# Performance work log

Measured on AMD Instinct MI355X. Metric: run time of the kernel, lower is better.

The kernel has to match this reference:

```python
import jax, jax.numpy as jnp
import numpy as np
from jax import lax

NUM_EXPERTS = 5
K = 3


def setup_inputs() -> dict:
    key = jax.random.key(0)
    ks = jax.random.split(key, 16)
    B = 8192
    d_in, d_h = 32 * 10 * 10, 128

    def w(k, shape, fan_in):
        return jax.random.normal(k, shape, jnp.float32) / np.sqrt(fan_in)

    return {
        "x": jax.random.normal(ks[0], (B, 1, 28, 28), jnp.float32),
        # conv feature extractor: 28 -> conv5 -> 24 -> pool2 -> 12 -> conv3 -> 10
        "conv1_w": w(ks[1], (16, 1, 5, 5), 25),
        "conv1_b": jnp.zeros((16,), jnp.float32),
        "conv2_w": w(ks[2], (32, 16, 3, 3), 16 * 9),
        "conv2_b": jnp.zeros((32,), jnp.float32),
        # top-k gate
        "gate_w": w(ks[3], (d_in, NUM_EXPERTS), d_in),
        "gate_b": jnp.zeros((NUM_EXPERTS,), jnp.float32),
        # 5 experts: Linear(3200,128)-Tanh-Linear(128,128)-Tanh, stacked on axis 0
        "e1_w": w(ks[4], (NUM_EXPERTS, d_in, d_h), d_in),
        "e1_b": jnp.zeros((NUM_EXPERTS, d_h), jnp.float32),
        "e2_w": w(ks[5], (NUM_EXPERTS, d_h, d_h), d_h),
        "e2_b": jnp.zeros((NUM_EXPERTS, d_h), jnp.float32),
        # softmax head
        "sm_w": w(ks[6], (d_h, 10), d_h),
        "sm_b": jnp.zeros((10,), jnp.float32),
    }


def _conv_features(x, c1w, c1b, c2w, c2b):
    dn = ("NCHW", "OIHW", "NCHW")
    h = lax.conv_general_dilated(x, c1w, (1, 1), "VALID", dimension_numbers=dn)
    h = jax.nn.relu(h + c1b[None, :, None, None])          # [B,16,24,24]
    h = lax.reduce_window(h, -jnp.inf, lax.max, (1, 1, 2, 2), (1, 1, 2, 2), "VALID")  # [B,16,12,12]
    h = lax.conv_general_dilated(h, c2w, (1, 1), "VALID", dimension_numbers=dn)
    h = jax.nn.relu(h + c2b[None, :, None, None])          # [B,32,10,10]
    return h.reshape(h.shape[0], -1)                       # [B,3200]


def reference(x, conv1_w, conv1_b, conv2_w, conv2_b, gate_w, gate_b,
              e1_w, e1_b, e2_w, e2_b, sm_w, sm_b):
    h = _conv_features(x, conv1_w, conv1_b, conv2_w, conv2_b)  # [B, 3200]
    B = h.shape[0]

    # token-choice top-K gating over NUM_EXPERTS experts
    probs = jax.nn.softmax(h @ gate_w + gate_b, axis=-1)       # [B, E]
    topv, topi = lax.top_k(probs, K)                           # [B, K]
    topv = topv / jnp.sum(topv, axis=-1, keepdims=True)        # renormalize
    w_full = jnp.zeros((B, NUM_EXPERTS), h.dtype).at[
        jnp.arange(B)[:, None], topi].set(topv)                # [B, E] sparse combine weights

    # expert MLPs (small, computed densely and masked by gate weights)
    h1 = jnp.tanh(jnp.einsum("bd,edh->ebh", h, e1_w) + e1_b[:, None, :])   # [E,B,128]
    h2 = jnp.tanh(jnp.einsum("ebh,ehk->ebk", h1, e2_w) + e2_b[:, None, :])  # [E,B,128]
    moe_out = jnp.einsum("be,ebk->bk", w_full, h2)             # weighted sum combine, [B,128]

    logits = moe_out @ sm_w + sm_b                             # [B,10]
    return jax.nn.softmax(logits, axis=1)
```

## Files before the change

### kernel.cpp

```cpp
#include <hip/hip_runtime.h>
#include <hip/hip_bf16.h>
#include <hip/hip_fp16.h>

#define NB 8192
#define D_IN 3200
#define D_H 128
#define NE 5

typedef _Float16 f16x8 __attribute__((ext_vector_type(8)));
typedef _Float16 f16x4 __attribute__((ext_vector_type(4)));
typedef float f32x4 __attribute__((ext_vector_type(4)));

__device__ __forceinline__ void gload16(const _Float16* g, _Float16* l) {
    __builtin_amdgcn_global_load_lds(
        (const __attribute__((address_space(1))) void*)g,
        (__attribute__((address_space(3))) void*)l, 16, 0, 0);
}

__global__ __launch_bounds__(256) void k_gwprep(const float* __restrict__ gw,
                                                float* __restrict__ gwC,
                                                int* __restrict__ cnt) {
    int i = blockIdx.x * 256 + threadIdx.x;
    if (i < 16000) {
        int e = i / 3200, rem = i - e * 3200;
        int o = rem >> 5, co = rem & 31;
        gwC[i] = gw[(co * 100 + o) * 5 + e];
    }
    if (blockIdx.x == 0 && threadIdx.x < NE) cnt[threadIdx.x] = 0;
}

#define PCL_S 24
__global__ __launch_bounds__(256, 3) void k_feat(
    const float* __restrict__ x, const float* __restrict__ c1w, const float* __restrict__ c1b,
    const float* __restrict__ c2w, const float* __restrict__ c2b,
    const float* __restrict__ gwC, const float* __restrict__ gb,
    const float* __restrict__ e1w, _Float16* __restrict__ wT,
    const float* __restrict__ e2w, _Float16* __restrict__ e2T,
    _Float16* __restrict__ h16, float* __restrict__ wfull)
{
    __shared__ union {
        struct {
            __align__(16) float xs[784];
            __align__(16) float c1wsP[448];
            __align__(16) _Float16 b2h[5120];
            __align__(16) _Float16 b2l[5120];
            __align__(16) _Float16 pclh[144 * PCL_S];
            __align__(16) _Float16 pcll[144 * PCL_S];
            float red[32];
        } f;
        float tile[64 * 65];
    } S;
    int bid = blockIdx.x;
    int t = threadIdx.x;

    if (bid < 520) {
        if (bid < 500) {
            int e = bid / 100, rem = bid - e * 100;
            int k0 = (rem >> 1) * 64, n0 = (rem & 1) * 64;
            const float* src = e1w + (size_t)e * D_IN * D_H;
            _Float16* dst = wT + (size_t)e * D_H * D_IN;
            for (int i = 0; i < 16; ++i) {
                int idx = t + i * 256;
                int kr = idx >> 6, nc = idx & 63;
                S.tile[kr * 65 + nc] = src[(size_t)(k0 + kr) * D_H + n0 + nc];
            }
            __syncthreads();
            for (int i = 0; i < 16; ++i) {
                int idx = t + i * 256;
                int nr = idx >> 6, kc = idx & 63;
                dst[(size_t)(n0 + nr) * D_IN + k0 + kc] = (_Float16)S.tile[kc * 65 + nr];
            }
        } else {
            int idx2 = bid - 500;
            int e = idx2 >> 2, rem = idx2 & 3;
            int k0 = (rem >> 1) * 64, n0 = (rem & 1) * 64;
            const float* src = e2w + (size_t)e * D_H * D_H;
            _Float16* dst = e2T + (size_t)e * D_H * D_H;
            for (int i = 0; i < 16; ++i) {
                int idx = t + i * 256;
                int kr = idx >> 6, nc = idx & 63;
                S.tile[kr * 65 + nc] = src[(size_t)(k0 + kr) * D_H + n0 + nc];
            }
            __syncthreads();
            for (int i = 0; i < 16; ++i) {
                int idx = t + i * 256;
                int nr = idx >> 6, kc = idx & 63;
                dst[(size_t)(n0 + nr) * D_H + k0 + kc] = (_Float16)S.tile[kc * 65 + nr];
            }
        }
        return;
    }

    int b = bid - 520;
    for (int i = t; i < 784; i += 256) S.f.xs[i] = x[(size_t)b * 784 + i];
    for (int i = t; i < 400; i += 256) {
        int c = i / 25, q = i - c * 25;
        S.f.c1wsP[c * 28 + q] = c1w[i];
    }
    for (int i = t; i < 5120; i += 256) {
        int co = i / 160, k = i - co * 160;
        int s = k >> 4, ci = k & 15;
        float v = (s == 9) ? 0.f : c2w[(co * 16 + ci) * 9 + s];
        _Float16 vh = (_Float16)v;
        S.f.b2h[i] = vh;
        S.f.b2l[i] = (_Float16)(v - (float)vh);
    }
    __syncthreads();

    {
        int c = t >> 4;
        int tile = t & 15;
        int tr = tile >> 2, tc = tile & 3;
        float w1r[25];
        #pragma unroll
        for (int q = 0; q < 6; ++q) {
            float4 v4 = *(const float4*)&S.f.c1wsP[c * 28 + q * 4];
            w1r[q * 4 + 0] = v4.x; w1r[q * 4 + 1] = v4.y;
            w1r[q * 4 + 2] = v4.z; w1r[q * 4 + 3] = v4.w;
        }
        w1r[24] = S.f.c1wsP[c * 28 + 24];
        float bias1 = c1b[c];
        float win[5][10];
        float pacc[3][3];
        #pragma unroll
        for (int i = 0; i < 3; ++i)
            #pragma unroll
            for (int j = 0; j < 3; ++j) pacc[i][j] = 0.f;
        int r0 = 6 * tr, col0 = 6 * tc;
        #pragma unroll
        for (int cr = 0; cr < 6; ++cr) {
            if (cr == 0) {
                #pragma unroll
                for (int rr = 0; rr < 5; ++rr)
                    #pragma unroll
                    for (int m = 0; m < 5; ++m) {
                        float2 v = *(const float2*)&S.f.xs[(r0 + rr) * 28 + col0 + 2 * m];
                        win[rr][2 * m] = v.x; win[rr][2 * m + 1] = v.y;
                    }
            } else {
                int dstr = (cr + 4) % 5;
                #pragma unroll
                for (int m = 0; m < 5; ++m) {
                    float2 v = *(const float2*)&S.f.xs[(r0 + cr + 4) * 28 + col0 + 2 * m];
                    win[dstr][2 * m] = v.x; win[dstr][2 * m + 1] = v.y;
                }
            }
            #pragma unroll
            for (int oc = 0; oc < 6; ++oc) {
                float s = bias1;
                #pragma unroll
                for (int u = 0; u < 5; ++u)
                    #pragma unroll
                    for (int v = 0; v < 5; ++v)
                        s += win[(cr + u) % 5][oc + v] * w1r[u * 5 + v];
                s = fmaxf(s, 0.f);
                pacc[cr >> 1][oc >> 1] = fmaxf(pacc[cr >> 1][oc >> 1], s);
            }
        }
        #pragma unroll
        for (int i = 0; i < 3; ++i)
            #pragma unroll
            for (int j = 0; j < 3; ++j) {
                int pos = (3 * tr + i) * 12 + (3 * tc + j);
                float v = pacc[i][j];
                _Float16 vh = (_Float16)v;
                S.f.pclh[pos * PCL_S + c] = vh;
                S.f.pcll[pos * PCL_S + c] = (_Float16)(v - (float)vh);
            }
    }
    __syncthreads();

    float part[5] = {0, 0, 0, 0, 0};
    int lane = t & 63, wv = t >> 6;
    int quad = lane >> 4, l16 = lane & 15;
    int quadh = quad >> 1, quadl = quad & 1;
    const int offA[5] = {0, 2, 13, 24, 26};
    const int offB[5] = {1, 12, 14, 25, 0};
    {
        int nt = wv & 1;
        int co = nt * 16 + l16;
        f16x8 bh[5], bl[5];
        #pragma unroll
        for (int kc = 0; kc < 5; ++kc) {
            bh[kc] = *(const f16x8*)&S.f.b2h[co * 160 + kc * 32 + quad * 8];
            bl[kc] = *(const f16x8*)&S.f.b2l[co * 160 + kc * 32 + quad * 8];
        }
        float bco = c2b[co];
        for (int mt = wv >> 1; mt < 7; mt += 2) {
            int o_a = mt * 16 + l16;
            int o_cl = o_a < 100 ? o_a : 99;
            int pb = (o_cl / 10) * 12 + (o_cl % 10);
            f32x4 acc = (f32x4){0.f, 0.f, 0.f, 0.f};
            #pragma unroll
            for (int kc = 0; kc < 5; ++kc) {
                int off = quadh ? offB[kc] : offA[kc];
                f16x8 ah = *(const f16x8*)&S.f.pclh[(pb + off) * PCL_S + quadl * 8];
                f16x8 al = *(const f16x8*)&S.f.pcll[(pb + off) * PCL_S + quadl * 8];
                acc = __builtin_amdgcn_mfma_f32_16x16x32_f16(ah, bh[kc], acc, 0, 0, 0);
                acc = __builtin_amdgcn_mfma_f32_16x16x32_f16(ah, bl[kc], acc, 0, 0, 0);
                acc = __builtin_amdgcn_mfma_f32_16x16x32_f16(al, bh[kc], acc, 0, 0, 0);
            }
            if (mt < 6 || quad == 0) {
                int o0 = mt * 16 + quad * 4;
                f16x4 st;
                #pragma unroll
                for (int r = 0; r < 4; ++r) {
                    float hv = fmaxf(acc[r] + bco, 0.f);
                    st[r] = (_Float16)hv;
                    #pragma unroll
                    for (int e = 0; e < 5; ++e)
                        part[e] += hv * gwC[e * 3200 + (o0 + r) * 32 + co];
                }
                *(f16x4*)&h16[(size_t)b * D_IN + co * 100 + o0] = st;
            }
        }
    }

    #pragma unroll
    for (int e = 0; e < 5; ++e) {
        float v = part[e];
        for (int off = 32; off > 0; off >>= 1) v += __shfl_down(v, off, 64);
        if (lane == 0) S.f.red[wv * 8 + e] = v;
    }
    __syncthreads();
    if (t == 0) {
        float lg[5], p[5];
        float mx = -1e30f;
        for (int e = 0; e < 5; ++e) {
            lg[e] = S.f.red[e] + S.f.red[8 + e] + S.f.red[16 + e] + S.f.red[24 + e] + gb[e];
            mx = fmaxf(mx, lg[e]);
        }
        float sum = 0.f;
        for (int e = 0; e < 5; ++e) { p[e] = expf(lg[e] - mx); sum += p[e]; }
        for (int e = 0; e < 5; ++e) p[e] /= sum;
        bool used[5] = {false, false, false, false, false};
        float out5[5] = {0, 0, 0, 0, 0};
        int ti[3]; float tv[3]; float tsum = 0.f;
        for (int jj = 0; jj < 3; ++jj) {
            int best = 0; float bv = -1.f;
            for (int e = 0; e < 5; ++e)
                if (!used[e] && p[e] > bv) { bv = p[e]; best = e; }
            used[best] = true; ti[jj] = best; tv[jj] = bv; tsum += bv;
        }
        for (int jj = 0; jj < 3; ++jj) out5[ti[jj]] = tv[jj] / tsum;
        for (int e = 0; e < 5; ++e) wfull[b * 5 + e] = out5[e];
    }
}

__global__ __launch_bounds__(256) void k_compact(
    const float* __restrict__ wfull, int* __restrict__ cnt, int* __restrict__ lists)
{
    int tok = blockIdx.x * 256 + threadIdx.x;
    int lane = threadIdx.x & 63;
    float w[5];
    #pragma unroll
    for (int e = 0; e < 5; ++e) w[e] = wfull[(size_t)tok * 5 + e];
    #pragma unroll
    for (int e = 0; e < 5; ++e) {
        bool sel = w[e] > 0.f;
        unsigned long long mask = __ballot(sel);
        int leader = __ffsll((long long)mask) - 1;
        int base = 0;
        if (lane == leader) base = atomicAdd(&cnt[e], __popcll(mask));
        base = __shfl(base, leader, 64);
        if (sel) {
            int pos = base + __popcll(mask & ((1ull << lane) - 1ull));
            lists[e * NB + pos] = tok;
        }
    }
}

#define H1S 136
union SLds {
    struct { _Float16 As0[2048]; _Float16 As1[2048];
             _Float16 Bs0[4096]; _Float16 Bs1[4096]; } p1;
    _Float16 e2ws[128 * H1S];
    _Float16 smwT[16 * 128];
};

__global__ __launch_bounds__(256, 3) void k_e1e2(
    const _Float16* __restrict__ h16, const _Float16* __restrict__ wT,
    const _Float16* __restrict__ e2T,
    const float* __restrict__ e1b, const float* __restrict__ e2b,
    const float* __restrict__ smw,
    const float* __restrict__ wfull, const int* __restrict__ cnt,
    const int* __restrict__ lists, float* __restrict__ logits)
{
    __shared__ SLds u;
    __shared__ __align__(16) _Float16 h1s[64 * H1S];
    __shared__ float wfl[64];
    __shared__ int rows[64];
    int bid = blockIdx.x;
    int e = bid >> 7;
    int mt = bid & 127;
    int cnt_e = cnt[e];
    int m0 = mt * 64;
    if (m0 >= cnt_e) return;
    int t = threadIdx.x;
    int lane = t & 63, wv = t >> 6;
    int waveM = wv >> 1, waveN = wv & 1;
    int quad = lane >> 4, l16 = lane & 15;
    if (t < 64) {
        int r = m0 + t;
        int row = (r < cnt_e) ? lists[e * NB + r] : lists[e * NB];
        rows[t] = row;
        wfl[t] = (r < cnt_e) ? wfull[(size_t)row * 5 + e] : 0.f;
    }
    __syncthreads();

    const _Float16* bbase = wT + (size_t)e * (D_H * D_IN);
    int srow = t >> 2;
    int scol = (t & 3) * 8;
    const _Float16* aptr = h16 + (size_t)rows[srow] * D_IN + scol;
    const _Float16* bptr0 = bbase + (size_t)srow * D_IN + scol;
    const _Float16* bptr1 = bbase + (size_t)(64 + srow) * D_IN + scol;
    f32x4 acc[2][4];
    #pragma unroll
    for (int i = 0; i < 2; ++i)
        #pragma unroll
        for (int j = 0; j < 4; ++j) acc[i][j] = (f32x4){0.f, 0.f, 0.f, 0.f};

    for (int k0 = 0; k0 < D_IN; k0 += 64) {
        gload16(aptr + k0,        u.p1.As0 + wv * 512);
        gload16(aptr + k0 + 32,   u.p1.As1 + wv * 512);
        gload16(bptr0 + k0,       u.p1.Bs0 + wv * 512);
        gload16(bptr0 + k0 + 32,  u.p1.Bs1 + wv * 512);
        gload16(bptr1 + k0,       u.p1.Bs0 + 2048 + wv * 512);
        gload16(bptr1 + k0 + 32,  u.p1.Bs1 + 2048 + wv * 512);
        __syncthreads();
        #pragma unroll
        for (int ch = 0; ch < 2; ++ch) {
            const _Float16* Ab = ch ? u.p1.As1 : u.p1.As0;
            const _Float16* Bb = ch ? u.p1.Bs1 : u.p1.Bs0;
            f16x8 af[2], bf[4];
            #pragma unroll
            for (int ms = 0; ms < 2; ++ms)
                af[ms] = *(const f16x8*)&Ab[(waveM * 32 + ms * 16 + l16) * 32 + quad * 8];
            #pragma unroll
            for (int ns = 0; ns < 4; ++ns)
                bf[ns] = *(const f16x8*)&Bb[(waveN * 64 + ns * 16 + l16) * 32 + quad * 8];
            #pragma unroll
            for (int ms = 0; ms < 2; ++ms)
                #pragma unroll
                for (int ns = 0; ns < 4; ++ns)
                    acc[ms][ns] = __builtin_amdgcn_mfma_f32_16x16x32_f16(af[ms], bf[ns], acc[ms][ns], 0, 0, 0);
        }
        __syncthreads();
    }

    #pragma unroll
    for (int ms = 0; ms < 2; ++ms) {
        int rbase = waveM * 32 + ms * 16 + quad * 4;
        #pragma unroll
        for (int ns = 0; ns < 4; ++ns) {
            int n = waveN * 64 + ns * 16 + l16;
            float bias = e1b[e * D_H + n];
            #pragma unroll
            for (int r = 0; r < 4; ++r)
                h1s[(rbase + r) * H1S + n] = (_Float16)tanhf(acc[ms][ns][r] + bias);
        }
    }
    __syncthreads();

    {
        int rr = t >> 1, cc = (t & 1) * 64;
        const _Float16* src = e2T + (size_t)e * (D_H * D_H) + (size_t)rr * D_H + cc;
        #pragma unroll
        for (int i = 0; i < 8; ++i)
            *(uint4*)&u.e2ws[rr * H1S + cc + i * 8] = *(const uint4*)(src + i * 8);
    }
    __syncthreads();

    f32x4 acc2[2][4];
    #pragma unroll
    for (int i = 0; i < 2; ++i)
        #pragma unroll
        for (int j = 0; j < 4; ++j) acc2[i][j] = (f32x4){0.f, 0.f, 0.f, 0.f};
    #pragma unroll
    for (int kc = 0; kc < 4; ++kc) {
        f16x8 a2[2], b2[4];
        #pragma unroll
        for (int ms = 0; ms < 2; ++ms)
            a2[ms] = *(const f16x8*)&h1s[(waveM * 32 + ms * 16 + l16) * H1S + kc * 32 + quad * 8];
        #pragma unroll
        for (int ns = 0; ns < 4; ++ns)
            b2[ns] = *(const f16x8*)&u.e2ws[(waveN * 64 + ns * 16 + l16) * H1S + kc * 32 + quad * 8];
        #pragma unroll
        for (int ms = 0; ms < 2; ++ms)
            #pragma unroll
            for (int ns = 0; ns < 4; ++ns)
                acc2[ms][ns] = __builtin_amdgcn_mfma_f32_16x16x32_f16(a2[ms], b2[ns], acc2[ms][ns], 0, 0, 0);
    }
    __syncthreads();

    for (int i = t; i < 2048; i += 256) {
        int n = i >> 7, k = i & 127;
        u.smwT[i] = (_Float16)(n < 10 ? smw[k * 10 + n] : 0.f);
    }
    #pragma unroll
    for (int ms = 0; ms < 2; ++ms) {
        int rbase = waveM * 32 + ms * 16 + quad * 4;
        #pragma unroll
        for (int ns = 0; ns < 4; ++ns) {
            int n = waveN * 64 + ns * 16 + l16;
            float bias = e2b[e * D_H + n];
            #pragma unroll
            for (int r = 0; r < 4; ++r) {
                int lrow = rbase + r;
                h1s[lrow * H1S + n] = (_Float16)(wfl[lrow] * tanhf(acc2[ms][ns][r] + bias));
            }
        }
    }
    __syncthreads();

    {
        f32x4 acc3 = (f32x4){0.f, 0.f, 0.f, 0.f};
        #pragma unroll
        for (int kc = 0; kc < 4; ++kc) {
            f16x8 a3 = *(const f16x8*)&h1s[(wv * 16 + l16) * H1S + kc * 32 + quad * 8];
            f16x8 b3 = *(const f16x8*)&u.smwT[l16 * 128 + kc * 32 + quad * 8];
            acc3 = __builtin_amdgcn_mfma_f32_16x16x32_f16(a3, b3, acc3, 0, 0, 0);
        }
        if (l16 < 10) {
            #pragma unroll
            for (int r = 0; r < 4; ++r) {
                int row = wv * 16 + quad * 4 + r;
                unsafeAtomicAdd(&logits[(size_t)rows[row] * 10 + l16], acc3[r]);
            }
        }
    }
}

__global__ __launch_bounds__(256) void k_smax(
    const float* __restrict__ logits, const float* __restrict__ smb,
    float* __restrict__ out)
{
    int r = blockIdx.x * 256 + threadIdx.x;
    float lg[10];
    float mx = -1e30f;
    #pragma unroll
    for (int c = 0; c < 10; ++c) {
        lg[c] = logits[(size_t)r * 10 + c] + smb[c];
        mx = fmaxf(mx, lg[c]);
    }
    float s = 0.f;
    #pragma unroll
    for (int c = 0; c < 10; ++c) { lg[c] = expf(lg[c] - mx); s += lg[c]; }
    float inv = 1.f / s;
    #pragma unroll
    for (int c = 0; c < 10; ++c) out[(size_t)r * 10 + c] = lg[c] * inv;
}

extern "C" void kernel_launch(void* const* d_in, const int* in_sizes, int n_in,
                              void* d_out, int out_size, void* d_ws, size_t ws_size,
                              hipStream_t stream)
{
    const float* x   = (const float*)d_in[0];
    const float* c1w = (const float*)d_in[1];
    const float* c1b = (const float*)d_in[2];
    const float* c2w = (const float*)d_in[3];
    const float* c2b = (const float*)d_in[4];
    const float* gw  = (const float*)d_in[5];
    const float* gb  = (const float*)d_in[6];
    const float* e1w = (const float*)d_in[7];
    const float* e1b = (const float*)d_in[8];
    const float* e2w = (const float*)d_in[9];
    const float* e2b = (const float*)d_in[10];
    const float* smw = (const float*)d_in[11];
    const float* smb = (const float*)d_in[12];
    float* out = (float*)d_out;

    char* ws = (char*)d_ws;
    size_t off = 0;
    auto alloc = [&](size_t bytes) {
        void* p = ws + off;
        off += (bytes + 255) & ~(size_t)255;
        return p;
    };
    _Float16* h16 = (_Float16*)alloc((size_t)NB * D_IN * 2);
    _Float16* wT  = (_Float16*)alloc((size_t)NE * D_H * D_IN * 2);
    _Float16* e2T = (_Float16*)alloc((size_t)NE * D_H * D_H * 2);
    float* wfull  = (float*)alloc((size_t)NB * NE * 4);
    float* logits = (float*)alloc((size_t)NB * 10 * 4);
    float* gwC    = (float*)alloc((size_t)NE * D_IN * 4);
    int* cnt      = (int*)alloc(NE * 4);
    int* lists    = (int*)alloc((size_t)NE * NB * 4);

    hipMemsetAsync(logits, 0, (size_t)NB * 10 * 4, stream);
    k_gwprep<<<dim3(63), 256, 0, stream>>>(gw, gwC, cnt);
    k_feat<<<dim3(520 + NB), 256, 0, stream>>>(x, c1w, c1b, c2w, c2b, gwC, gb,
                                               e1w, wT, e2w, e2T, h16, wfull);
    k_compact<<<dim3(NB / 256), 256, 0, stream>>>(wfull, cnt, lists);
    k_e1e2<<<dim3(128 * NE), 256, 0, stream>>>(h16, wT, e2T, e1b, e2b, smw,
                                               wfull, cnt, lists, logits);
    k_smax<<<dim3(NB / 256), 256, 0, stream>>>(logits, smb, out);
}
```

Baseline: 309.4 us.

## Precompute conv weight layouts once and shrink per-block LDS in feature kernel

New measurement: 346.1 us. 1.12x slower.

```diff
diff --git a/kernel.cpp b/kernel.cpp
--- a/kernel.cpp
+++ b/kernel.cpp
@@ -17,23 +17,42 @@
         (__attribute__((address_space(3))) void*)l, 16, 0, 0);
 }
 
-__global__ __launch_bounds__(256) void k_gwprep(const float* __restrict__ gw,
-                                                float* __restrict__ gwC,
-                                                int* __restrict__ cnt) {
+__global__ __launch_bounds__(256) void k_prep(const float* __restrict__ gw,
+                                              const float* __restrict__ c2w,
+                                              const float* __restrict__ c1w,
+                                              float* __restrict__ gwC8,
+                                              _Float16* __restrict__ b2g,
+                                              float* __restrict__ c1wP,
+                                              int* __restrict__ cnt) {
     int i = blockIdx.x * 256 + threadIdx.x;
-    if (i < 16000) {
-        int e = i / 3200, rem = i - e * 3200;
-        int o = rem >> 5, co = rem & 31;
-        gwC[i] = gw[(co * 100 + o) * 5 + e];
+    if (i < 25600) {
+        int idx = i >> 3, e = i & 7;
+        int o = idx >> 5, co = idx & 31;
+        gwC8[i] = (e < 5) ? gw[(co * 100 + o) * 5 + e] : 0.f;
+    } else if (i < 30720) {
+        int j = i - 25600;
+        int co = j / 160, k = j - co * 160;
+        int s = k >> 4, ci = k & 15;
+        float v = (s == 9) ? 0.f : c2w[(co * 16 + ci) * 9 + s];
+        _Float16 vh = (_Float16)v;
+        int kc = k >> 5, w = k & 31, quad = w >> 3, r = w & 7;
+        int base = ((co * 5 + kc) * 4 + quad) * 16 + r;
+        b2g[base] = vh;
+        b2g[base + 8] = (_Float16)(v - (float)vh);
+    } else if (i < 31120) {
+        int j = i - 30720;
+        int c = j / 25, q = j - c * 25;
+        c1wP[c * 28 + q] = c1w[j];
     }
     if (blockIdx.x == 0 && threadIdx.x < NE) cnt[threadIdx.x] = 0;
 }
 
 #define PCL_S 24
-__global__ __launch_bounds__(256, 3) void k_feat(
-    const float* __restrict__ x, const float* __restrict__ c1w, const float* __restrict__ c1b,
-    const float* __restrict__ c2w, const float* __restrict__ c2b,
-    const float* __restrict__ gwC, const float* __restrict__ gb,
+__global__ __launch_bounds__(256, 6) void k_feat(
+    const float* __restrict__ x, const float* __restrict__ c1b,
+    const float* __restrict__ c2b,
+    const float* __restrict__ c1wP, const _Float16* __restrict__ b2g,
+    const float* __restrict__ gwC8, const float* __restrict__ gb,
     const float* __restrict__ e1w, _Float16* __restrict__ wT,
     const float* __restrict__ e2w, _Float16* __restrict__ e2T,
     _Float16* __restrict__ h16, float* __restrict__ wfull)
@@ -41,9 +60,6 @@
     __shared__ union {
         struct {
             __align__(16) float xs[784];
-            __align__(16) float c1wsP[448];
-            __align__(16) _Float16 b2h[5120];
-            __align__(16) _Float16 b2l[5120];
             __align__(16) _Float16 pclh[144 * PCL_S];
             __align__(16) _Float16 pcll[144 * PCL_S];
             float red[32];
@@ -92,20 +108,13 @@
     }
 
     int b = bid - 520;
-    for (int i = t; i < 784; i += 256) S.f.xs[i] = x[(size_t)b * 784 + i];
-    for (int i = t; i < 400; i += 256) {
-        int c = i / 25, q = i - c * 25;
-        S.f.c1wsP[c * 28 + q] = c1w[i];
-    }
-    for (int i = t; i < 5120; i += 256) {
-        int co = i / 160, k = i - co * 160;
-        int s = k >> 4, ci = k & 15;
-        float v = (s == 9) ? 0.f : c2w[(co * 16 + ci) * 9 + s];
-        _Float16 vh = (_Float16)v;
-        S.f.b2h[i] = vh;
-        S.f.b2l[i] = (_Float16)(v - (float)vh);
-    }
-    __syncthreads();
+    if (t < 196)
+        *(float4*)&S.f.xs[t * 4] = *(const float4*)&x[(size_t)b * 784 + t * 4];
+    __syncthreads();
+
+    int lane = t & 63, wv = t >> 6;
+    int quad = lane >> 4, l16 = lane & 15;
+    int quadh = quad >> 1, quadl = quad & 1;
 
     {
         int c = t >> 4;
@@ -114,11 +123,11 @@
         float w1r[25];
         #pragma unroll
         for (int q = 0; q < 6; ++q) {
-            float4 v4 = *(const float4*)&S.f.c1wsP[c * 28 + q * 4];
+            float4 v4 = *(const float4*)&c1wP[c * 28 + q * 4];
             w1r[q * 4 + 0] = v4.x; w1r[q * 4 + 1] = v4.y;
             w1r[q * 4 + 2] = v4.z; w1r[q * 4 + 3] = v4.w;
         }
-        w1r[24] = S.f.c1wsP[c * 28 + 24];
+        w1r[24] = c1wP[c * 28 + 24];
         float bias1 = c1b[c];
         float win[5][10];
         float pacc[3][3];
@@ -168,51 +177,52 @@
                 S.f.pcll[pos * PCL_S + c] = (_Float16)(v - (float)vh);
             }
     }
+
+    int nt = wv & 1;
+    int co = nt * 16 + l16;
+    f16x8 bh[5], bl[5];
+    #pragma unroll
+    for (int kc = 0; kc < 5; ++kc) {
+        const _Float16* p = b2g + ((co * 5 + kc) * 4 + quad) * 16;
+        bh[kc] = *(const f16x8*)p;
+        bl[kc] = *(const f16x8*)(p + 8);
+    }
+    float bco = c2b[co];
     __syncthreads();
 
     float part[5] = {0, 0, 0, 0, 0};
-    int lane = t & 63, wv = t >> 6;
-    int quad = lane >> 4, l16 = lane & 15;
-    int quadh = quad >> 1, quadl = quad & 1;
     const int offA[5] = {0, 2, 13, 24, 26};
     const int offB[5] = {1, 12, 14, 25, 0};
-    {
-        int nt = wv & 1;
-        int co = nt * 16 + l16;
-        f16x8 bh[5], bl[5];
+    for (int mt = wv >> 1; mt < 7; mt += 2) {
+        int o_a = mt * 16 + l16;
+        int o_cl = o_a < 100 ? o_a : 99;
+        int pb = (o_cl / 10) * 12 + (o_cl % 10);
+        f32x4 acc = (f32x4){0.f, 0.f, 0.f, 0.f};
         #pragma unroll
         for (int kc = 0; kc < 5; ++kc) {
-            bh[kc] = *(const f16x8*)&S.f.b2h[co * 160 + kc * 32 + quad * 8];
-            bl[kc] = *(const f16x8*)&S.f.b2l[co * 160 + kc * 32 + quad * 8];
-        }
-        float bco = c2b[co];
-        for (int mt = wv >> 1; mt < 7; mt += 2) {
-            int o_a = mt * 16 + l16;
-            int o_cl = o_a < 100 ? o_a : 99;
-            int pb = (o_cl / 10) * 12 + (o_cl % 10);
-            f32x4 acc = (f32x4){0.f, 0.f, 0.f, 0.f};
-            #pragma unroll
-            for (int kc = 0; kc < 5; ++kc) {
-                int off = quadh ? offB[kc] : offA[kc];
-                f16x8 ah = *(const f16x8*)&S.f.pclh[(pb + off) * PCL_S + quadl * 8];
-                f16x8 al = *(const f16x8*)&S.f.pcll[(pb + off) * PCL_S + quadl * 8];
-                acc = __builtin_amdgcn_mfma_f32_16x16x32_f16(ah, bh[kc], acc, 0, 0, 0);
-                acc = __builtin_amdgcn_mfma_f32_16x16x32_f16(ah, bl[kc], acc, 0, 0, 0);
-                acc = __builtin_amdgcn_mfma_f32_16x16x32_f16(al, bh[kc], acc, 0, 0, 0);
-            }
-            if (mt < 6 || quad == 0) {
-                int o0 = mt * 16 + quad * 4;
-                f16x4 st;
-                #pragma unroll
-                for (int r = 0; r < 4; ++r) {
-                    float hv = fmaxf(acc[r] + bco, 0.f);
-                    st[r] = (_Float16)hv;
-                    #pragma unroll
-                    for (int e = 0; e < 5; ++e)
-                        part[e] += hv * gwC[e * 3200 + (o0 + r) * 32 + co];
-                }
-                *(f16x4*)&h16[(size_t)b * D_IN + co * 100 + o0] = st;
-            }
+            int off = quadh ? offB[kc] : offA[kc];
+            f16x8 ah = *(const f16x8*)&S.f.pclh[(pb + off) * PCL_S + quadl * 8];
+            f16x8 al = *(const f16x8*)&S.f.pcll[(pb + off) * PCL_S + quadl * 8];
+            acc = __builtin_amdgcn_mfma_f32_16x16x32_f16(ah, bh[kc], acc, 0, 0, 0);
+            acc = __builtin_amdgcn_mfma_f32_16x16x32_f16(ah, bl[kc], acc, 0, 0, 0);
+            acc = __builtin_amdgcn_mfma_f32_16x16x32_f16(al, bh[kc], acc, 0, 0, 0);
+        }
+        if (mt < 6 || quad == 0) {
+            int o0 = mt * 16 + quad * 4;
+            f16x4 st;
+            #pragma unroll
+            for (int r = 0; r < 4; ++r) {
+                float hv = fmaxf(acc[r] + bco, 0.f);
+                st[r] = (_Float16)hv;
+                int idx = (o0 + r) * 32 + co;
+                const f32x4 g0 = *(const f32x4*)&gwC8[(size_t)idx * 8];
+                part[0] += hv * g0[0];
+                part[1] += hv * g0[1];
+                part[2] += hv * g0[2];
+                part[3] += hv * g0[3];
+                part[4] += hv * gwC8[(size_t)idx * 8 + 4];
+            }
+            *(f16x4*)&h16[(size_t)b * D_IN + co * 100 + o0] = st;
         }
     }
 
@@ -482,13 +492,15 @@
     _Float16* e2T = (_Float16*)alloc((size_t)NE * D_H * D_H * 2);
     float* wfull  = (float*)alloc((size_t)NB * NE * 4);
     float* logits = (float*)alloc((size_t)NB * 10 * 4);
-    float* gwC    = (float*)alloc((size_t)NE * D_IN * 4);
+    float* gwC8   = (float*)alloc((size_t)25600 * 4);
+    _Float16* b2g = (_Float16*)alloc((size_t)10240 * 2);
+    float* c1wP   = (float*)alloc((size_t)448 * 4);
     int* cnt      = (int*)alloc(NE * 4);
     int* lists    = (int*)alloc((size_t)NE * NB * 4);
 
     hipMemsetAsync(logits, 0, (size_t)NB * 10 * 4, stream);
-    k_gwprep<<<dim3(63), 256, 0, stream>>>(gw, gwC, cnt);
-    k_feat<<<dim3(520 + NB), 256, 0, stream>>>(x, c1w, c1b, c2w, c2b, gwC, gb,
+    k_prep<<<dim3(122), 256, 0, stream>>>(gw, c2w, c1w, gwC8, b2g, c1wP, cnt);
+    k_feat<<<dim3(520 + NB), 256, 0, stream>>>(x, c1b, c2b, c1wP, b2g, gwC8, gb,
                                                e1w, wT, e2w, e2T, h16, wfull);
     k_compact<<<dim3(NB / 256), 256, 0, stream>>>(wfull, cnt, lists);
     k_e1e2<<<dim3(128 * NE), 256, 0, stream>>>(h16, wT, e2T, e1b, e2b, smw,
```

## Double-buffer expert-1 GEMM LDS tiles and alias h1s into the union

Applied to the files above, without the earlier changes.

Result: no change. 304.8 us (-1.5%).

```diff
diff --git a/kernel.cpp b/kernel.cpp
--- a/kernel.cpp
+++ b/kernel.cpp
@@ -271,11 +271,12 @@
 }
 
 #define H1S 136
-union SLds {
-    struct { _Float16 As0[2048]; _Float16 As1[2048];
-             _Float16 Bs0[4096]; _Float16 Bs1[4096]; } p1;
-    _Float16 e2ws[128 * H1S];
-    _Float16 smwT[16 * 128];
+union __align__(16) SLds {
+    struct { _Float16 As0[2048], As1[2048], Bs0[4096], Bs1[4096]; } p[2];
+    struct {
+        __align__(16) _Float16 h1s[64 * H1S];
+        __align__(16) _Float16 e2ws[128 * H1S];
+    } q;
 };
 
 __global__ __launch_bounds__(256, 3) void k_e1e2(
@@ -287,7 +288,6 @@
     const int* __restrict__ lists, float* __restrict__ logits)
 {
     __shared__ SLds u;
-    __shared__ __align__(16) _Float16 h1s[64 * H1S];
     __shared__ float wfl[64];
     __shared__ int rows[64];
     int bid = blockIdx.x;
@@ -320,18 +320,33 @@
         #pragma unroll
         for (int j = 0; j < 4; ++j) acc[i][j] = (f32x4){0.f, 0.f, 0.f, 0.f};
 
-    for (int k0 = 0; k0 < D_IN; k0 += 64) {
-        gload16(aptr + k0,        u.p1.As0 + wv * 512);
-        gload16(aptr + k0 + 32,   u.p1.As1 + wv * 512);
-        gload16(bptr0 + k0,       u.p1.Bs0 + wv * 512);
-        gload16(bptr0 + k0 + 32,  u.p1.Bs1 + wv * 512);
-        gload16(bptr1 + k0,       u.p1.Bs0 + 2048 + wv * 512);
-        gload16(bptr1 + k0 + 32,  u.p1.Bs1 + 2048 + wv * 512);
-        __syncthreads();
+    _Float16* bufc = (_Float16*)&u.p[0];
+    _Float16* bufn = (_Float16*)&u.p[1];
+    #define STAGE(base, kk)                                           \
+        do {                                                          \
+            gload16(aptr  + (kk),        (base) + 0    + wv * 512);   \
+            gload16(aptr  + (kk) + 32,   (base) + 2048 + wv * 512);   \
+            gload16(bptr0 + (kk),        (base) + 4096 + wv * 512);   \
+            gload16(bptr0 + (kk) + 32,   (base) + 8192 + wv * 512);   \
+            gload16(bptr1 + (kk),        (base) + 4096 + 2048 + wv * 512); \
+            gload16(bptr1 + (kk) + 32,   (base) + 8192 + 2048 + wv * 512); \
+        } while (0)
+
+    STAGE(bufc, 0);
+    const int NT = D_IN / 64;
+    for (int it = 0; it < NT; ++it) {
+        if (it + 1 < NT) {
+            STAGE(bufn, (it + 1) * 64);
+            asm volatile("s_waitcnt vmcnt(6)" ::: "memory");
+        } else {
+            asm volatile("s_waitcnt vmcnt(0)" ::: "memory");
+        }
+        __builtin_amdgcn_s_barrier();
+        __builtin_amdgcn_sched_barrier(0);
         #pragma unroll
         for (int ch = 0; ch < 2; ++ch) {
-            const _Float16* Ab = ch ? u.p1.As1 : u.p1.As0;
-            const _Float16* Bb = ch ? u.p1.Bs1 : u.p1.Bs0;
+            const _Float16* Ab = bufc + (ch ? 2048 : 0);
+            const _Float16* Bb = bufc + 4096 + (ch ? 4096 : 0);
             f16x8 af[2], bf[4];
             #pragma unroll
             for (int ms = 0; ms < 2; ++ms)
@@ -345,8 +360,10 @@
                 for (int ns = 0; ns < 4; ++ns)
                     acc[ms][ns] = __builtin_amdgcn_mfma_f32_16x16x32_f16(af[ms], bf[ns], acc[ms][ns], 0, 0, 0);
         }
-        __syncthreads();
-    }
+        __builtin_amdgcn_s_barrier();
+        _Float16* tmp = bufc; bufc = bufn; bufn = tmp;
+    }
+    #undef STAGE
 
     #pragma unroll
     for (int ms = 0; ms < 2; ++ms) {
@@ -357,7 +374,7 @@
             float bias = e1b[e * D_H + n];
             #pragma unroll
             for (int r = 0; r < 4; ++r)
-                h1s[(rbase + r) * H1S + n] = (_Float16)tanhf(acc[ms][ns][r] + bias);
+                u.q.h1s[(rbase + r) * H1S + n] = (_Float16)tanhf(acc[ms][ns][r] + bias);
         }
     }
     __syncthreads();
@@ -367,7 +384,7 @@
         const _Float16* src = e2T + (size_t)e * (D_H * D_H) + (size_t)rr * D_H + cc;
         #pragma unroll
         for (int i = 0; i < 8; ++i)
-            *(uint4*)&u.e2ws[rr * H1S + cc + i * 8] = *(const uint4*)(src + i * 8);
+            *(uint4*)&u.q.e2ws[rr * H1S + cc + i * 8] = *(const uint4*)(src + i * 8);
     }
     __syncthreads();
 
@@ -381,10 +398,10 @@
         f16x8 a2[2], b2[4];
         #pragma unroll
         for (int ms = 0; ms < 2; ++ms)
-            a2[ms] = *(const f16x8*)&h1s[(waveM * 32 + ms * 16 + l16) * H1S + kc * 32 + quad * 8];
+            a2[ms] = *(const f16x8*)&u.q.h1s[(waveM * 32 + ms * 16 + l16) * H1S + kc * 32 + quad * 8];
         #pragma unroll
         for (int ns = 0; ns < 4; ++ns)
-            b2[ns] = *(const f16x8*)&u.e2ws[(waveN * 64 + ns * 16 + l16) * H1S + kc * 32 + quad * 8];
+            b2[ns] = *(const f16x8*)&u.q.e2ws[(waveN * 64 + ns * 16 + l16) * H1S + kc * 32 + quad * 8];
         #pragma unroll
         for (int ms = 0; ms < 2; ++ms)
             #pragma unroll
@@ -393,9 +410,10 @@
     }
     __syncthreads();
 
+    _Float16* smwT = u.q.e2ws;
     for (int i = t; i < 2048; i += 256) {
         int n = i >> 7, k = i & 127;
-        u.smwT[i] = (_Float16)(n < 10 ? smw[k * 10 + n] : 0.f);
+        smwT[i] = (_Float16)(n < 10 ? smw[k * 10 + n] : 0.f);
     }
     #pragma unroll
     for (int ms = 0; ms < 2; ++ms) {
@@ -407,7 +425,7 @@
             #pragma unroll
             for (int r = 0; r < 4; ++r) {
                 int lrow = rbase + r;
-                h1s[lrow * H1S + n] = (_Float16)(wfl[lrow] * tanhf(acc2[ms][ns][r] + bias));
+                u.q.h1s[lrow * H1S + n] = (_Float16)(wfl[lrow] * tanhf(acc2[ms][ns][r] + bias));
             }
         }
     }
@@ -417,8 +435,8 @@
         f32x4 acc3 = (f32x4){0.f, 0.f, 0.f, 0.f};
         #pragma unroll
         for (int kc = 0; kc < 4; ++kc) {
-            f16x8 a3 = *(const f16x8*)&h1s[(wv * 16 + l16) * H1S + kc * 32 + quad * 8];
-            f16x8 b3 = *(const f16x8*)&u.smwT[l16 * 128 + kc * 32 + quad * 8];
+            f16x8 a3 = *(const f16x8*)&u.q.h1s[(wv * 16 + l16) * H1S + kc * 32 + quad * 8];
+            f16x8 b3 = *(const f16x8*)&smwT[l16 * 128 + kc * 32 + quad * 8];
             acc3 = __builtin_amdgcn_mfma_f32_16x16x32_f16(a3, b3, acc3, 0, 0, 0);
         }
         if (l16 < 10) {
```
